# Performance work log

Hardware: AMD Instinct MI355X
Metric: run time of the kernel (lower is better)

Reference implementation:

```python
import jax, jax.numpy as jnp
import numpy as np

NMS_PRE, NMS_POST, NMS_THRESH = 1024, 512, 0.7
B, A, FEAT = 4, 70400, 27648
BN_EPS = 1e-5


def _bev_iou(boxes):
    # boxes: [K, 7] (x, y, z, dx, dy, dz, ry); axis-aligned BEV IoU
    x, y, dx, dy = boxes[:, 0], boxes[:, 1], boxes[:, 3], boxes[:, 4]
    x1, x2 = x - 0.5 * dx, x + 0.5 * dx
    y1, y2 = y - 0.5 * dy, y + 0.5 * dy
    iw = jnp.clip(jnp.minimum(x2[:, None], x2[None, :]) - jnp.maximum(x1[:, None], x1[None, :]), 0.0)
    ih = jnp.clip(jnp.minimum(y2[:, None], y2[None, :]) - jnp.maximum(y1[:, None], y1[None, :]), 0.0)
    inter = iw * ih
    area = dx * dy
    return inter / jnp.clip(area[:, None] + area[None, :] - inter, 1e-6)


def _greedy_nms(boxes, thresh):
    # boxes sorted by score desc; returns keep mask [K]
    K = boxes.shape[0]
    iou = _bev_iou(boxes)
    idx = jnp.arange(K)

    def step(keep, i):
        sup = (iou[i] > thresh) & (idx > i) & keep[i]
        return keep & ~sup, None

    keep, _ = jax.lax.scan(step, jnp.ones(K, dtype=bool), jnp.arange(K))
    return keep


def _proposal_one(box, cls):
    # box: [A, 7], cls: [A, n_cls]  ->  padded rois [NPOST,7], scores [NPOST], labels [NPOST]
    score = jnp.max(cls, axis=-1)
    label = jnp.argmax(cls, axis=-1)
    top_score, top_idx = jax.lax.top_k(score, NMS_PRE)
    top_box = box[top_idx]
    keep = _greedy_nms(top_box, NMS_THRESH)
    # stable: kept entries first, preserving score order
    order = jnp.argsort(jnp.where(keep, jnp.arange(NMS_PRE), NMS_PRE + jnp.arange(NMS_PRE)))
    sel = order[:NMS_POST]
    valid = jnp.arange(NMS_POST) < jnp.minimum(jnp.sum(keep), NMS_POST)
    rois = jnp.where(valid[:, None], top_box[sel], 0.0)
    roi_score = jnp.where(valid, top_score[sel], 0.0)
    roi_label = jnp.where(valid, label[top_idx][sel], 0) + 1  # +1 as in module
    return rois, roi_score, roi_label


def _bn_relu(h, g, b):
    # eval-mode BN with running_mean=0, running_var=1
    return jax.nn.relu(h * (g / jnp.sqrt(1.0 + BN_EPS)) + b)


def _decode(reg, anchors):
    # ResidualCoder_v1.decode_torch
    xa, ya, za = anchors[..., 0], anchors[..., 1], anchors[..., 2]
    dxa, dya, dza, ra = anchors[..., 3], anchors[..., 4], anchors[..., 5], anchors[..., 6]
    xt, yt, zt = reg[..., 0], reg[..., 1], reg[..., 2]
    dxt, dyt, dzt, rt = reg[..., 3], reg[..., 4], reg[..., 5], reg[..., 6]
    diag = jnp.sqrt(dxa * dxa + dya * dya)
    return jnp.stack([
        xt * diag + xa, yt * diag + ya, zt * dza + za,
        jnp.exp(dxt) * dxa, jnp.exp(dyt) * dya, jnp.exp(dzt) * dza,
        rt + ra], axis=-1)


def _rotate_z(box, ang):
    # rotate x,y of box [..., 7] by ang [...]
    c, s = jnp.cos(ang), jnp.sin(ang)
    x = box[..., 0] * c - box[..., 1] * s
    y = box[..., 0] * s + box[..., 1] * c
    return jnp.concatenate([x[..., None], y[..., None], box[..., 2:]], axis=-1)


def reference(rpn_box_preds, rpn_cls_preds, pooled_features,
              Ws1, g1, b1, Ws2, g2, b2,
              Wc1, gc1, bc1, Wc2, gc2, bc2, Wc3, bc3,
              Wr1, gr1, br1, Wr2, gr2, br2, Wr3, br3):
    # proposal_layer: per-batch topk + NMS + padded scatter (vmapped)
    rois, roi_scores, roi_labels = jax.vmap(_proposal_one)(rpn_box_preds, rpn_cls_preds)

    # shared / cls / reg heads (1x1 Conv1d == per-roi MLP), dropout off (eval)
    x = _bn_relu(pooled_features @ Ws1.T, g1, b1)
    x = _bn_relu(x @ Ws2.T, g2, b2)
    c = _bn_relu(x @ Wc1.T, gc1, bc1)
    c = _bn_relu(c @ Wc2.T, gc2, bc2)
    cls_preds = c @ Wc3.T + bc3          # [B*NPOST, 1]
    r = _bn_relu(x @ Wr1.T, gr1, br1)
    r = _bn_relu(r @ Wr2.T, gr2, br2)
    reg_preds = r @ Wr3.T + br3          # [B*NPOST, 7]

    bsz = rois.shape[0]
    cls_preds = cls_preds.reshape(bsz, -1, cls_preds.shape[-1])
    reg_preds = reg_preds.reshape(bsz, -1, 7)

    # generate_predict_box: decode against detached rois with xyz zeroed
    anchors = jax.lax.stop_gradient(rois)
    anchors = anchors.at[..., 0:3].set(0.0)
    box_ct = _decode(reg_preds, anchors)
    box_preds = _rotate_z(box_ct, rois[..., 6])
    box_preds = jnp.concatenate([box_preds[..., 0:3] + rois[..., 0:3], box_preds[..., 3:]], axis=-1)

    return jnp.concatenate([cls_preds, box_preds, roi_scores[..., None]], axis=-1)  # [B, NPOST, 9]


def setup_inputs():
    key = jax.random.key(0)
    ks = jax.random.split(key, 32)
    u = jax.random.uniform(ks[0], (B, A, 7), dtype=jnp.float32)
    lo = jnp.array([0.0, -40.0, -2.0, 1.5, 1.4, 1.0, -3.14159], jnp.float32)
    hi = jnp.array([70.0, 40.0, 0.0, 4.5, 2.0, 2.0, 3.14159], jnp.float32)
    rpn_box_preds = lo + u * (hi - lo)
    rpn_cls_preds = jax.random.normal(ks[1], (B, A, 3), dtype=jnp.float32)
    pooled_features = jax.random.normal(ks[2], (B * NMS_POST, FEAT), dtype=jnp.float32) * 0.1

    def w(k, o, i, std=None):
        s = (1.0 / np.sqrt(i)) if std is None else std
        return jax.random.normal(k, (o, i), dtype=jnp.float32) * s

    d = dict(
        rpn_box_preds=rpn_box_preds, rpn_cls_preds=rpn_cls_preds, pooled_features=pooled_features,
        Ws1=w(ks[3], 256, FEAT), g1=jnp.ones(256), b1=jnp.zeros(256),
        Ws2=w(ks[4], 256, 256), g2=jnp.ones(256), b2=jnp.zeros(256),
        Wc1=w(ks[5], 256, 256), gc1=jnp.ones(256), bc1=jnp.zeros(256),
        Wc2=w(ks[6], 256, 256), gc2=jnp.ones(256), bc2=jnp.zeros(256),
        Wc3=w(ks[7], 1, 256), bc3=jnp.zeros(1),
        Wr1=w(ks[8], 256, 256), gr1=jnp.ones(256), br1=jnp.zeros(256),
        Wr2=w(ks[9], 256, 256), gr2=jnp.ones(256), br2=jnp.zeros(256),
        Wr3=w(ks[10], 7, 256, std=0.001), br3=jnp.zeros(7),
    )
    return d
```

## Files before the change

### kernel.cpp

```cpp
#include <hip/hip_runtime.h>
#include <cstdint>

typedef unsigned int u32;
typedef unsigned long long u64;
typedef unsigned short u16;

#define BATCH 4
#define A_CNT 70400
#define FEAT 27648
#define KSPLIT 16
#define KCHUNK 1728
#define NTILE_IT 27

typedef __attribute__((ext_vector_type(8))) short bf16x8;
typedef __attribute__((ext_vector_type(4))) float f32x4;
typedef __attribute__((ext_vector_type(2))) u32 u32x2;
typedef __attribute__((ext_vector_type(4))) u32 u32x4;

constexpr size_t OF_KEYS = 0;
constexpr size_t OF_TBOX = OF_KEYS + 1126400;
constexpr size_t OF_TSC  = OF_TBOX + 114688;
constexpr size_t OF_BX1  = OF_TSC + 16384;
constexpr size_t OF_BX2  = OF_BX1 + 16384;
constexpr size_t OF_BY1  = OF_BX2 + 16384;
constexpr size_t OF_BY2  = OF_BY1 + 16384;
constexpr size_t OF_BAR  = OF_BY2 + 16384;
constexpr size_t OF_MASK = OF_BAR + 16384;
constexpr size_t OF_ROIS = OF_MASK + 524288;
constexpr size_t OF_RSC  = OF_ROIS + 57344;
constexpr size_t OF_BSW  = OF_RSC + 8192;
constexpr size_t OF_PART = OF_BSW + 14155776;
constexpr size_t WS_NEED = OF_PART + 33554432;

__device__ __forceinline__ u32 keyOf(float f) {
  u32 u = __float_as_uint(f);
  return (u & 0x80000000u) ? ~u : (u | 0x80000000u);
}
__device__ __forceinline__ float keyToF(u32 k) {
  u32 u = (k & 0x80000000u) ? (k ^ 0x80000000u) : ~k;
  return __uint_as_float(u);
}
__device__ __forceinline__ u16 f2bf(float f) {
  u32 u = __float_as_uint(f);
  u32 r = 0x7FFFu + ((u >> 16) & 1u);
  return (u16)((u + r) >> 16);
}
__device__ __forceinline__ void gload_lds16(const void* g, void* l) {
  auto gp = reinterpret_cast<const __attribute__((address_space(1))) unsigned int*>(
      reinterpret_cast<uintptr_t>(g));
  auto lp = reinterpret_cast<__attribute__((address_space(3))) unsigned int*>(
      reinterpret_cast<uintptr_t>(l));
  __builtin_amdgcn_global_load_lds(gp, lp, 16, 0, 0);
}
__device__ __forceinline__ u64 shflx64(u64 v, int m) {
  u32 lo = (u32)v, hi = (u32)(v >> 32);
  lo = __shfl_xor(lo, m, 64);
  hi = __shfl_xor(hi, m, 64);
  return ((u64)hi << 32) | lo;
}
__device__ __forceinline__ u32x4 pack8(float4 a, float4 b) {
  u32x4 o;
  o.x = (u32)f2bf(a.x) | ((u32)f2bf(a.y) << 16);
  o.y = (u32)f2bf(a.z) | ((u32)f2bf(a.w) << 16);
  o.z = (u32)f2bf(b.x) | ((u32)f2bf(b.y) << 16);
  o.w = (u32)f2bf(b.z) | ((u32)f2bf(b.w) << 16);
  return o;
}

__global__ __launch_bounds__(1024) void k_fatA(const float* __restrict__ cls,
    const float* __restrict__ Ws1, u32* __restrict__ keys, u32* __restrict__ Bsw)
{
  int bid = blockIdx.x;
  int t = threadIdx.x;
  if (bid < 864) {
    u32 w = (u32)bid * 1024u + t;
    u32 tile = w >> 11;
    u32 rem = w & 2047u;
    u32 n = rem >> 3;
    u32 pq = (rem & 7u) << 4;
    u32 q0 = pq ^ ((n & 7u) << 4);
    u32 col0 = tile * 64u + (q0 >> 1);
    const float* src = Ws1 + (size_t)n * FEAT + col0;
    float4 f0 = *(const float4*)src;
    float4 f1 = *(const float4*)(src + 4);
    ((u32x4*)Bsw)[w] = pack8(f0, f1);
    return;
  }
  u32 g = (u32)(bid - 864) * 1024u + t;
  float s0 = cls[(size_t)g * 3 + 0];
  float s1 = cls[(size_t)g * 3 + 1];
  float s2 = cls[(size_t)g * 3 + 2];
  keys[g] = keyOf(fmaxf(s0, fmaxf(s1, s2)));
}

__global__ __launch_bounds__(1024) void k_big(const u32* __restrict__ keys,
    const float* __restrict__ boxes, const float* __restrict__ A,
    const u32* __restrict__ Bsw, float* __restrict__ part,
    float* __restrict__ tbox, float* __restrict__ tsc,
    float* __restrict__ bx1, float* __restrict__ bx2, float* __restrict__ by1,
    float* __restrict__ by2, float* __restrict__ bar)
{
  __shared__ __align__(16) char smem[81920];
  int bid = blockIdx.x;
  int t = threadIdx.x;
  if (bid < 4) {
    int b = bid;
    int lane = t & 63, wv = t >> 6;
    const u32* kb = keys + (size_t)b * A_CNT;
    u64* s = (u64*)smem;
    u32* partials = (u32*)(smem + 16384);
    u32* ccp = (u32*)(smem + 16448);
    u32 h[35];
#pragma unroll
    for (int j = 0; j < 35; ++j) {
      int g0 = t + ((2 * j) << 10);
      int g1 = t + ((2 * j + 1) << 10);
      u32 a = (g0 < A_CNT) ? (kb[g0] >> 16) : 0u;
      u32 c2 = (g1 < A_CNT) ? (kb[g1] >> 16) : 0u;
      h[j] = a | (c2 << 16);
    }
    if (t == 0) ccp[0] = 0u;
    u32 lo = 0, hi = 65536;
    while (hi - lo > 1) {
      u32 mid = (lo + hi) >> 1;
      u32 c = 0;
#pragma unroll
      for (int j = 0; j < 35; ++j) {
        c += ((h[j] & 0xFFFFu) >= mid) ? 1u : 0u;
        c += ((h[j] >> 16) >= mid) ? 1u : 0u;
      }
#pragma unroll
      for (int o = 32; o > 0; o >>= 1) c += __shfl_xor(c, o, 64);
      __syncthreads();
      if (lane == 0) partials[wv] = c;
      __syncthreads();
      u32 tot = 0;
#pragma unroll
      for (int w2 = 0; w2 < 16; ++w2) tot += partials[w2];
      if (tot >= 1024u) lo = mid; else hi = mid;
    }
    u32 kth = lo;
    __syncthreads();
    u32 kc = kb[t];
#pragma unroll 1
    for (int i = 0; i < 69; ++i) {
      int g = t + (i << 10);
      u32 k = kc;
      if (i < 68) {
        int gn = t + ((i + 1) << 10);
        kc = (gn < A_CNT) ? kb[gn] : 0u;
      }
      bool pass = (g < A_CNT) && ((k >> 16) >= kth);
      u64 mm = __ballot(pass);
      if (mm) {
        int leader = __ffsll((unsigned long long)mm) - 1;
        u32 base = 0;
        if (lane == leader) base = atomicAdd(ccp, (u32)__popcll(mm));
        base = __shfl(base, leader, 64);
        if (pass) {
          u32 pos = base + (u32)__popcll(mm & ((1ull << lane) - 1ull));
          if (pos < 2048u) s[pos] = ((u64)k << 32) | (u32)(~(u32)g);
        }
      }
    }
    __syncthreads();
    u32 m = ccp[0]; if (m > 2048u) m = 2048u;
    for (int e = t; e < 2048; e += 1024) if (e >= (int)m) s[e] = 0ull;
    __syncthreads();
    {
      u64 v0 = s[2 * t], v1 = s[2 * t + 1];
#pragma unroll
      for (u32 k = 2; k <= 128; k <<= 1) {
        bool desc = ((t & (k >> 1)) == 0);
#pragma unroll
        for (u32 j = (k >> 1); j >= 2; j >>= 1) {
          u32 mmk = j >> 1;
          u64 p0 = shflx64(v0, mmk);
          u64 p1 = shflx64(v1, mmk);
          bool up = ((t & mmk) == 0);
          bool mx = (desc == up);
          v0 = mx ? (v0 > p0 ? v0 : p0) : (v0 < p0 ? v0 : p0);
          v1 = mx ? (v1 > p1 ? v1 : p1) : (v1 < p1 ? v1 : p1);
        }
        if (desc ? (v0 < v1) : (v0 > v1)) { u64 tmp = v0; v0 = v1; v1 = tmp; }
      }
      s[2 * t] = v0; s[2 * t + 1] = v1;
      __syncthreads();
      for (u32 k = 256; k <= 2048; k <<= 1) {
        for (u32 j = k >> 1; j >= 128; j >>= 1) {
          for (int e = t; e < 2048; e += 1024) {
            u32 p = (u32)e ^ j;
            if (p > (u32)e) {
              bool d2 = ((e & k) == 0);
              u64 x = s[e], y = s[p];
              if (d2 ? (x < y) : (x > y)) { s[e] = y; s[p] = x; }
            }
          }
          __syncthreads();
        }
        u64 v0 = s[2 * t], v1 = s[2 * t + 1];
        bool desc = ((t & (k >> 1)) == 0);
#pragma unroll
        for (u32 j = 64; j >= 2; j >>= 1) {
          u32 mmk = j >> 1;
          u64 p0 = shflx64(v0, mmk);
          u64 p1 = shflx64(v1, mmk);
          bool up = ((t & mmk) == 0);
          bool mx = (desc == up);
          v0 = mx ? (v0 > p0 ? v0 : p0) : (v0 < p0 ? v0 : p0);
          v1 = mx ? (v1 > p1 ? v1 : p1) : (v1 < p1 ? v1 : p1);
        }
        if (desc ? (v0 < v1) : (v0 > v1)) { u64 tmp = v0; v0 = v1; v1 = tmp; }
        s[2 * t] = v0; s[2 * t + 1] = v1;
        __syncthreads();
      }
    }
    u64 comp = s[t];
    u32 kk = (u32)(comp >> 32);
    u32 a = ~(u32)(comp & 0xFFFFFFFFull);
    int o = b * 1024 + t;
    tsc[o] = keyToF(kk);
    const float* bp = boxes + ((size_t)b * A_CNT + a) * 7;
    float x = bp[0], y = bp[1], z = bp[2], dx = bp[3], dy = bp[4], dz = bp[5], rr = bp[6];
    float* tb = tbox + (size_t)o * 7;
    tb[0] = x; tb[1] = y; tb[2] = z; tb[3] = dx; tb[4] = dy; tb[5] = dz; tb[6] = rr;
    {
#pragma clang fp contract(off)
      bx1[o] = x - 0.5f * dx; bx2[o] = x + 0.5f * dx;
      by1[o] = y - 0.5f * dy; by2[o] = y + 0.5f * dy;
      bar[o] = dx * dy;
    }
    return;
  }
  int bid2 = bid - 4;
  int q = bid2 >> 3;
  int ks = (bid2 & 7) * 2 + (q >> 5);
  int mt = q & 31;
  int lane = t & 63, wvid = t >> 6;
  int row16 = lane & 15, kgrp = lane >> 4;

  f32x4 acc[4];
#pragma unroll
  for (int i = 0; i < 4; ++i) acc[i] = (f32x4){0.f, 0.f, 0.f, 0.f};

  int arow = t >> 4;
  const float* ap_base = A + ((size_t)(mt * 64 + arow)) * FEAT + (size_t)ks * KCHUNK + (t & 15) * 4;
  int asw = (arow & 7) << 4;
  int awoff = arow * 128 + (((t & 15) * 8) ^ asw);
  const char* bsrc_base = (const char*)Bsw + ((size_t)(ks * NTILE_IT)) * 32768 + wvid * 2048 + lane * 16;
  int bdoff = wvid * 2048 + lane * 16;
  char* Abase = smem;
  char* Bbase = smem + 16384;

  int aoff[4][2], boff[2];
#pragma unroll
  for (int ksub = 0; ksub < 2; ++ksub) {
    int qq = ksub * 64 + kgrp * 16;
#pragma unroll
    for (int mf = 0; mf < 4; ++mf) {
      int row = mf * 16 + row16;
      aoff[mf][ksub] = row * 128 + (qq ^ ((row & 7) << 4));
    }
    int n = wvid * 16 + row16;
    boff[ksub] = n * 128 + (qq ^ ((n & 7) << 4));
  }

  {
    float4 ga = *(const float4*)ap_base;
    u32x2 c;
    c.x = (u32)f2bf(ga.x) | ((u32)f2bf(ga.y) << 16);
    c.y = (u32)f2bf(ga.z) | ((u32)f2bf(ga.w) << 16);
    *(u32x2*)(Abase + awoff) = c;
    gload_lds16(bsrc_base, Bbase + bdoff);
    gload_lds16(bsrc_base + 1024, Bbase + bdoff + 1024);
  }
  __syncthreads();

  for (int it = 0; it < NTILE_IT; ++it) {
    char* Acur = Abase + ((it & 1) ? 8192 : 0);
    char* Anxt = Abase + ((it & 1) ? 0 : 8192);
    char* Bcur = Bbase + ((it & 1) ? 32768 : 0);
    char* Bnxt = Bbase + ((it & 1) ? 0 : 32768);
    bool has = (it + 1 < NTILE_IT);
    float4 ga;
    if (has) {
      ga = *(const float4*)(ap_base + (it + 1) * 64);
      const char* bs = bsrc_base + (size_t)(it + 1) * 32768;
      gload_lds16(bs, Bnxt + bdoff);
      gload_lds16(bs + 1024, Bnxt + bdoff + 1024);
    }
    bf16x8 bf0 = *(const bf16x8*)(Bcur + boff[0]);
    bf16x8 bf1 = *(const bf16x8*)(Bcur + boff[1]);
#pragma unroll
    for (int mf = 0; mf < 4; ++mf) {
      bf16x8 a0 = *(const bf16x8*)(Acur + aoff[mf][0]);
      acc[mf] = __builtin_amdgcn_mfma_f32_16x16x32_bf16(a0, bf0, acc[mf], 0, 0, 0);
      bf16x8 a1 = *(const bf16x8*)(Acur + aoff[mf][1]);
      acc[mf] = __builtin_amdgcn_mfma_f32_16x16x32_bf16(a1, bf1, acc[mf], 0, 0, 0);
    }
    if (has) {
      u32x2 c;
      c.x = (u32)f2bf(ga.x) | ((u32)f2bf(ga.y) << 16);
      c.y = (u32)f2bf(ga.z) | ((u32)f2bf(ga.w) << 16);
      *(u32x2*)(Anxt + awoff) = c;
    }
    __syncthreads();
  }
  float* pb = part + (size_t)ks * 524288;
#pragma unroll
  for (int mf = 0; mf < 4; ++mf) {
    int orow = mt * 64 + mf * 16 + kgrp * 4;
    int col = wvid * 16 + row16;
#pragma unroll
    for (int rr = 0; rr < 4; ++rr)
      pb[(size_t)(orow + rr) * 256 + col] = acc[mf][rr];
  }
}

__global__ __launch_bounds__(1024) void k_mask(const float* __restrict__ bx1,
    const float* __restrict__ bx2, const float* __restrict__ by1,
    const float* __restrict__ by2, const float* __restrict__ bar,
    u32* __restrict__ mask)
{
  __shared__ float csm[16][5][64];
  int tt = threadIdx.x;
  int ug = tt >> 6, ln = tt & 63;
  int unit = blockIdx.x * 16 + ug;
  int b = unit >> 8, cbk = (unit >> 4) & 15, rb = unit & 15;
  int o = b * 1024, jc0 = cbk * 64;
  int r = rb * 64 + ln;
  csm[ug][0][ln] = bx1[o + jc0 + ln];
  csm[ug][1][ln] = bx2[o + jc0 + ln];
  csm[ug][2][ln] = by1[o + jc0 + ln];
  csm[ug][3][ln] = by2[o + jc0 + ln];
  csm[ug][4][ln] = bar[o + jc0 + ln];
  __syncthreads();
  float rx1 = bx1[o + r], rx2 = bx2[o + r], ry1 = by1[o + r], ry2 = by2[o + r], rar = bar[o + r];
  u32 w0 = 0, w1 = 0;
  {
#pragma clang fp contract(off)
    for (int c = 0; c < 64; ++c) {
      int jc = jc0 + c;
      float iw = fminf(rx2, csm[ug][1][c]) - fmaxf(rx1, csm[ug][0][c]); iw = fmaxf(iw, 0.0f);
      float ih = fminf(ry2, csm[ug][3][c]) - fmaxf(ry1, csm[ug][2][c]); ih = fmaxf(ih, 0.0f);
      float inter = iw * ih;
      float den = fmaxf(rar + csm[ug][4][c] - inter, 1e-6f);
      float iou = inter / den;
      if ((iou > 0.7f) && (jc > r)) {
        if (c < 32) w0 |= 1u << c; else w1 |= 1u << (c - 32);
      }
    }
  }
  mask[((size_t)(o + r)) * 32 + cbk * 2 + 0] = w0;
  mask[((size_t)(o + r)) * 32 + cbk * 2 + 1] = w1;
}

__global__ __launch_bounds__(64) void k_nms(const u32* __restrict__ mask,
    const float* __restrict__ tbox, const float* __restrict__ tsc,
    float* __restrict__ rois, float* __restrict__ rsc)
{
  int b = blockIdx.x;
  int lane = threadIdx.x;
  int el = lane & 31;
  const u32* M = mask + (size_t)b * 1024 * 32;
  u32 R = 0;
  u32 cur[32], nxt[32];
#pragma unroll
  for (int i = 0; i < 32; ++i) cur[i] = M[(size_t)(i * 32 + el)];
#pragma unroll 1
  for (int c = 0; c < 32; ++c) {
    if (c < 31) {
      int nb = (c + 1) * 1024 + el;
#pragma unroll
      for (int i = 0; i < 32; ++i) nxt[i] = M[(size_t)(nb + i * 32)];
    }
    u32 w = R;
#pragma unroll
    for (int i = 0; i < 32; ++i) w |= ((w >> i) & 1u) ? 0u : cur[i];
    u32 wfin = __shfl(w, c, 64);
#pragma unroll
    for (int i = 0; i < 32; ++i) R |= ((wfin >> i) & 1u) ? 0u : cur[i];
#pragma unroll
    for (int i = 0; i < 32; ++i) cur[i] = nxt[i];
  }
  u32 keepw = (lane < 32) ? ~R : 0u;
  int c = __popc(keepw);
  int pre = c;
  for (int d = 1; d < 64; d <<= 1) {
    int v = __shfl_up(pre, d, 64);
    if (lane >= d) pre += v;
  }
  int total = __shfl(pre, 31, 64);
  int base = pre - c;
  if (lane < 32) {
    u32 w = keepw;
    int rank = base;
    while (w) {
      int bit = __ffs(w) - 1;
      w &= w - 1;
      if (rank < 512) {
        int r = lane * 32 + bit;
        const float* tb = tbox + ((size_t)b * 1024 + r) * 7;
        float* rp = rois + ((size_t)b * 512 + rank) * 7;
        rp[0] = tb[0]; rp[1] = tb[1]; rp[2] = tb[2]; rp[3] = tb[3];
        rp[4] = tb[4]; rp[5] = tb[5]; rp[6] = tb[6];
        rsc[b * 512 + rank] = tsc[b * 1024 + r];
      }
      rank++;
    }
  }
  for (int z = total + lane; z < 512; z += 64) {
    float* rp = rois + ((size_t)b * 512 + z) * 7;
    rp[0] = rp[1] = rp[2] = rp[3] = rp[4] = rp[5] = rp[6] = 0.0f;
    rsc[b * 512 + z] = 0.0f;
  }
}

__device__ __forceinline__ void layer4(const float (*IN)[256], const float* __restrict__ W,
    const float* __restrict__ g, const float* __restrict__ bb, float (*OUT)[256], int t, int h)
{
  float acc[4] = {0, 0, 0, 0};
  const float* Wrow = W + (size_t)t * 256;
  for (int k = 0; k < 256; k += 4) {
    float4 w4 = *(const float4*)&Wrow[k];
#pragma unroll
    for (int r = 0; r < 4; ++r) {
      float4 xv = *(const float4*)&IN[h * 4 + r][k];
      acc[r] = fmaf(xv.x, w4.x, acc[r]);
      acc[r] = fmaf(xv.y, w4.y, acc[r]);
      acc[r] = fmaf(xv.z, w4.z, acc[r]);
      acc[r] = fmaf(xv.w, w4.w, acc[r]);
    }
  }
  float sc = g[t] / sqrtf(1.0f + 1e-5f);
  float bv = bb[t];
#pragma unroll
  for (int r = 0; r < 4; ++r)
    OUT[h * 4 + r][t] = fmaxf(fmaf(acc[r], sc, bv), 0.0f);
}

__global__ __launch_bounds__(512) void k_chain(const float* __restrict__ part,
    const float* __restrict__ Ws2, const float* __restrict__ Wc1, const float* __restrict__ Wc2,
    const float* __restrict__ Wr1, const float* __restrict__ Wr2,
    const float* __restrict__ g1, const float* __restrict__ b1,
    const float* __restrict__ g2, const float* __restrict__ b2,
    const float* __restrict__ gc1, const float* __restrict__ bc1,
    const float* __restrict__ gc2, const float* __restrict__ bc2,
    const float* __restrict__ gr1, const float* __restrict__ br1,
    const float* __restrict__ gr2, const float* __restrict__ br2,
    const float* __restrict__ Wc3, const float* __restrict__ bc3,
    const float* __restrict__ Wr3, const float* __restrict__ br3,
    const float* __restrict__ rois, const float* __restrict__ rsc,
    float* __restrict__ out)
{
  int bid = blockIdx.x, tid = threadIdx.x;
  int t = tid & 255, h = tid >> 8;
  __shared__ __align__(16) float bufX[8][256];
  __shared__ __align__(16) float bufY[8][256];
  __shared__ __align__(16) float bufC[8][256];
  __shared__ __align__(16) float bufR[8][256];
  __shared__ float hd[64];
  {
    float sc = g1[t] / sqrtf(1.0f + 1e-5f);
    float bv = b1[t];
#pragma unroll
    for (int r = 0; r < 4; ++r) {
      int row = h * 4 + r;
      float s = 0.f;
#pragma unroll
      for (int ks = 0; ks < KSPLIT; ++ks)
        s += part[(size_t)ks * 524288 + (size_t)(bid * 8 + row) * 256 + t];
      bufX[row][t] = fmaxf(fmaf(s, sc, bv), 0.0f);
    }
  }
  __syncthreads();
  layer4(bufX, Ws2, g2, b2, bufY, t, h);
  __syncthreads();
  layer4(bufY, Wc1, gc1, bc1, bufC, t, h);
  layer4(bufY, Wr1, gr1, br1, bufR, t, h);
  __syncthreads();
  layer4(bufC, Wc2, gc2, bc2, bufX, t, h);
  layer4(bufR, Wr2, gr2, br2, bufY, t, h);
  __syncthreads();
  int wv = tid >> 6, ln = tid & 63;
  for (int task = wv; task < 64; task += 8) {
    float p;
    if (task < 8) {
      float4 yv = *(const float4*)&bufX[task][ln * 4];
      float4 w4 = ((const float4*)Wc3)[ln];
      p = yv.x * w4.x + yv.y * w4.y + yv.z * w4.z + yv.w * w4.w;
    } else {
      int i = task - 8, row = i / 7, j = i % 7;
      float4 yv = *(const float4*)&bufY[row][ln * 4];
      float4 w4 = ((const float4*)(Wr3 + j * 256))[ln];
      p = yv.x * w4.x + yv.y * w4.y + yv.z * w4.z + yv.w * w4.w;
    }
#pragma unroll
    for (int off = 32; off > 0; off >>= 1) p += __shfl_xor(p, off, 64);
    if (ln == 0) hd[task] = p;
  }
  __syncthreads();
  if (tid < 8) {
    int m = bid * 8 + tid;
    float clsv = hd[tid] + bc3[0];
    float rg[7];
#pragma unroll
    for (int j = 0; j < 7; ++j) rg[j] = hd[8 + tid * 7 + j] + br3[j];
    const float* R = rois + (size_t)m * 7;
    float rx = R[0], ry = R[1], rz = R[2], dxa = R[3], dya = R[4], dza = R[5], ra = R[6];
    float diag = sqrtf(dxa * dxa + dya * dya);
    float x = rg[0] * diag, y = rg[1] * diag, z = rg[2] * dza;
    float ex = expf(rg[3]) * dxa, ey = expf(rg[4]) * dya, ez = expf(rg[5]) * dza;
    float hr = rg[6] + ra;
    float cc = cosf(ra), sn = sinf(ra);
    float xr = x * cc - y * sn, yr = x * sn + y * cc;
    float* O = out + (size_t)m * 9;
    O[0] = clsv; O[1] = xr + rx; O[2] = yr + ry; O[3] = z + rz;
    O[4] = ex; O[5] = ey; O[6] = ez; O[7] = hr; O[8] = rsc[m];
  }
}

extern "C" void kernel_launch(void* const* d_in, const int* in_sizes, int n_in,
                              void* d_out, int out_size, void* d_ws, size_t ws_size,
                              hipStream_t stream)
{
  const float* rpn_box = (const float*)d_in[0];
  const float* rpn_cls = (const float*)d_in[1];
  const float* pooled  = (const float*)d_in[2];
  const float* Ws1 = (const float*)d_in[3];
  const float* g1  = (const float*)d_in[4];
  const float* b1  = (const float*)d_in[5];
  const float* Ws2 = (const float*)d_in[6];
  const float* g2  = (const float*)d_in[7];
  const float* b2  = (const float*)d_in[8];
  const float* Wc1 = (const float*)d_in[9];
  const float* gc1 = (const float*)d_in[10];
  const float* bc1 = (const float*)d_in[11];
  const float* Wc2 = (const float*)d_in[12];
  const float* gc2 = (const float*)d_in[13];
  const float* bc2 = (const float*)d_in[14];
  const float* Wc3 = (const float*)d_in[15];
  const float* bc3 = (const float*)d_in[16];
  const float* Wr1 = (const float*)d_in[17];
  const float* gr1 = (const float*)d_in[18];
  const float* br1 = (const float*)d_in[19];
  const float* Wr2 = (const float*)d_in[20];
  const float* gr2 = (const float*)d_in[21];
  const float* br2 = (const float*)d_in[22];
  const float* Wr3 = (const float*)d_in[23];
  const float* br3 = (const float*)d_in[24];

  if (ws_size < WS_NEED) return;

  char* ws = (char*)d_ws;
  u32* keys = (u32*)(ws + OF_KEYS);
  float* tbox = (float*)(ws + OF_TBOX);
  float* tsc  = (float*)(ws + OF_TSC);
  float* bx1 = (float*)(ws + OF_BX1);
  float* bx2 = (float*)(ws + OF_BX2);
  float* by1 = (float*)(ws + OF_BY1);
  float* by2 = (float*)(ws + OF_BY2);
  float* bar = (float*)(ws + OF_BAR);
  u32* mask = (u32*)(ws + OF_MASK);
  float* roisb = (float*)(ws + OF_ROIS);
  float* rscb  = (float*)(ws + OF_RSC);
  u32* Bsw = (u32*)(ws + OF_BSW);
  float* part = (float*)(ws + OF_PART);

  k_fatA<<<1139, 1024, 0, stream>>>(rpn_cls, Ws1, keys, Bsw);
  k_big<<<516, 1024, 0, stream>>>(keys, rpn_box, pooled, Bsw, part,
                                  tbox, tsc, bx1, bx2, by1, by2, bar);
  k_mask<<<64, 1024, 0, stream>>>(bx1, bx2, by1, by2, bar, mask);
  k_nms<<<4, 64, 0, stream>>>(mask, tbox, tsc, roisb, rscb);
  k_chain<<<256, 512, 0, stream>>>(part, Ws2, Wc1, Wc2, Wr1, Wr2,
                                   g1, b1, g2, b2, gc1, bc1, gc2, bc2,
                                   gr1, br1, gr2, br2, Wc3, bc3, Wr3, br3,
                                   roisb, rscb, (float*)d_out);
}
```

Measured before the change: 251.7 us.

## Enlarge GEMM block tile to 128 rows with 2x4 MFMA fragments per wave

The split-K GEMM blocks in k_big now cover 128 rows of pooled features instead of 64. Each wave computes a 32x64 output sub-tile (2x4 MFMA fragments) rather than 16x64, so every B tile loaded into LDS is reused across twice as many rows. This halves the number of GEMM blocks, and with them the redundant B-matrix global-to-LDS traffic. The cost is more accumulator registers, more LDS (96KB), and fewer blocks (256 GEMM blocks), which can reduce occupancy and parallelism across the GPU.

```diff
diff --git a/kernel.cpp b/kernel.cpp
--- a/kernel.cpp
+++ b/kernel.cpp
@@ -100,7 +100,7 @@
     float* __restrict__ bx1, float* __restrict__ bx2, float* __restrict__ by1,
     float* __restrict__ by2, float* __restrict__ bar)
 {
-  __shared__ __align__(16) char smem[81920];
+  __shared__ __align__(16) char smem[98304];
   int bid = blockIdx.x;
   int t = threadIdx.x;
   if (bid < 4) {
@@ -234,86 +234,96 @@
   }
   int bid2 = bid - 4;
   int q = bid2 >> 3;
-  int ks = (bid2 & 7) * 2 + (q >> 5);
-  int mt = q & 31;
+  int ks = (bid2 & 7) * 2 + (q >> 4);
+  int mt = q & 15;
   int lane = t & 63, wvid = t >> 6;
   int row16 = lane & 15, kgrp = lane >> 4;
-
-  f32x4 acc[4];
-#pragma unroll
-  for (int i = 0; i < 4; ++i) acc[i] = (f32x4){0.f, 0.f, 0.f, 0.f};
-
-  int arow = t >> 4;
-  const float* ap_base = A + ((size_t)(mt * 64 + arow)) * FEAT + (size_t)ks * KCHUNK + (t & 15) * 4;
+  int gm = wvid >> 2, gn = wvid & 3;
+
+  f32x4 acc[2][4];
+#pragma unroll
+  for (int i = 0; i < 2; ++i)
+#pragma unroll
+    for (int j = 0; j < 4; ++j) acc[i][j] = (f32x4){0.f, 0.f, 0.f, 0.f};
+
+  int arow = t >> 3;
+  const float* ap_base = A + ((size_t)(mt * 128 + arow)) * FEAT + (size_t)ks * KCHUNK + (t & 7) * 8;
   int asw = (arow & 7) << 4;
-  int awoff = arow * 128 + (((t & 15) * 8) ^ asw);
+  int awoff = arow * 128 + (((t & 7) * 16) ^ asw);
   const char* bsrc_base = (const char*)Bsw + ((size_t)(ks * NTILE_IT)) * 32768 + wvid * 2048 + lane * 16;
   int bdoff = wvid * 2048 + lane * 16;
   char* Abase = smem;
-  char* Bbase = smem + 16384;
-
-  int aoff[4][2], boff[2];
+  char* Bbase = smem + 32768;
+
+  int aoff[2][2], boff[4][2];
 #pragma unroll
   for (int ksub = 0; ksub < 2; ++ksub) {
     int qq = ksub * 64 + kgrp * 16;
 #pragma unroll
-    for (int mf = 0; mf < 4; ++mf) {
-      int row = mf * 16 + row16;
+    for (int mf = 0; mf < 2; ++mf) {
+      int row = gm * 32 + mf * 16 + row16;
       aoff[mf][ksub] = row * 128 + (qq ^ ((row & 7) << 4));
     }
-    int n = wvid * 16 + row16;
-    boff[ksub] = n * 128 + (qq ^ ((n & 7) << 4));
+#pragma unroll
+    for (int nf = 0; nf < 4; ++nf) {
+      int n = gn * 64 + nf * 16 + row16;
+      boff[nf][ksub] = n * 128 + (qq ^ ((n & 7) << 4));
+    }
   }
 
   {
-    float4 ga = *(const float4*)ap_base;
-    u32x2 c;
-    c.x = (u32)f2bf(ga.x) | ((u32)f2bf(ga.y) << 16);
-    c.y = (u32)f2bf(ga.z) | ((u32)f2bf(ga.w) << 16);
-    *(u32x2*)(Abase + awoff) = c;
+    const float4* ap = (const float4*)ap_base;
+    float4 ga0 = ap[0], ga1 = ap[1];
+    *(u32x4*)(Abase + awoff) = pack8(ga0, ga1);
     gload_lds16(bsrc_base, Bbase + bdoff);
     gload_lds16(bsrc_base + 1024, Bbase + bdoff + 1024);
   }
   __syncthreads();
 
   for (int it = 0; it < NTILE_IT; ++it) {
-    char* Acur = Abase + ((it & 1) ? 8192 : 0);
-    char* Anxt = Abase + ((it & 1) ? 0 : 8192);
+    char* Acur = Abase + ((it & 1) ? 16384 : 0);
+    char* Anxt = Abase + ((it & 1) ? 0 : 16384);
     char* Bcur = Bbase + ((it & 1) ? 32768 : 0);
     char* Bnxt = Bbase + ((it & 1) ? 0 : 32768);
     bool has = (it + 1 < NTILE_IT);
-    float4 ga;
+    float4 ga0, ga1;
     if (has) {
-      ga = *(const float4*)(ap_base + (it + 1) * 64);
+      const float4* ap = (const float4*)(ap_base + (it + 1) * 64);
+      ga0 = ap[0]; ga1 = ap[1];
       const char* bs = bsrc_base + (size_t)(it + 1) * 32768;
       gload_lds16(bs, Bnxt + bdoff);
       gload_lds16(bs + 1024, Bnxt + bdoff + 1024);
     }
-    bf16x8 bf0 = *(const bf16x8*)(Bcur + boff[0]);
-    bf16x8 bf1 = *(const bf16x8*)(Bcur + boff[1]);
-#pragma unroll
-    for (int mf = 0; mf < 4; ++mf) {
-      bf16x8 a0 = *(const bf16x8*)(Acur + aoff[mf][0]);
-      acc[mf] = __builtin_amdgcn_mfma_f32_16x16x32_bf16(a0, bf0, acc[mf], 0, 0, 0);
-      bf16x8 a1 = *(const bf16x8*)(Acur + aoff[mf][1]);
-      acc[mf] = __builtin_amdgcn_mfma_f32_16x16x32_bf16(a1, bf1, acc[mf], 0, 0, 0);
-    }
-    if (has) {
-      u32x2 c;
-      c.x = (u32)f2bf(ga.x) | ((u32)f2bf(ga.y) << 16);
-      c.y = (u32)f2bf(ga.z) | ((u32)f2bf(ga.w) << 16);
-      *(u32x2*)(Anxt + awoff) = c;
-    }
+    bf16x8 af[2][2], bf[4][2];
+#pragma unroll
+    for (int ksub = 0; ksub < 2; ++ksub) {
+#pragma unroll
+      for (int mf = 0; mf < 2; ++mf) af[mf][ksub] = *(const bf16x8*)(Acur + aoff[mf][ksub]);
+#pragma unroll
+      for (int nf = 0; nf < 4; ++nf) bf[nf][ksub] = *(const bf16x8*)(Bcur + boff[nf][ksub]);
+    }
+#pragma unroll
+    for (int ksub = 0; ksub < 2; ++ksub)
+#pragma unroll
+      for (int mf = 0; mf < 2; ++mf)
+#pragma unroll
+        for (int nf = 0; nf < 4; ++nf)
+          acc[mf][nf] = __builtin_amdgcn_mfma_f32_16x16x32_bf16(af[mf][ksub], bf[nf][ksub], acc[mf][nf], 0, 0, 0);
+    if (has)
+      *(u32x4*)(Anxt + awoff) = pack8(ga0, ga1);
     __syncthreads();
   }
   float* pb = part + (size_t)ks * 524288;
 #pragma unroll
-  for (int mf = 0; mf < 4; ++mf) {
-    int orow = mt * 64 + mf * 16 + kgrp * 4;
-    int col = wvid * 16 + row16;
-#pragma unroll
-    for (int rr = 0; rr < 4; ++rr)
-      pb[(size_t)(orow + rr) * 256 + col] = acc[mf][rr];
+  for (int mf = 0; mf < 2; ++mf) {
+    int orow = mt * 128 + gm * 32 + mf * 16 + kgrp * 4;
+#pragma unroll
+    for (int nf = 0; nf < 4; ++nf) {
+      int col = gn * 64 + nf * 16 + row16;
+#pragma unroll
+      for (int rr = 0; rr < 4; ++rr)
+        pb[(size_t)(orow + rr) * 256 + col] = acc[mf][nf][rr];
+    }
   }
 }
 
@@ -568,7 +578,7 @@
   float* part = (float*)(ws + OF_PART);
 
   k_fatA<<<1139, 1024, 0, stream>>>(rpn_cls, Ws1, keys, Bsw);
-  k_big<<<516, 1024, 0, stream>>>(keys, rpn_box, pooled, Bsw, part,
+  k_big<<<260, 1024, 0, stream>>>(keys, rpn_box, pooled, Bsw, part,
                                   tbox, tsc, bx1, bx2, by1, by2, bar);
   k_mask<<<64, 1024, 0, stream>>>(bx1, bx2, by1, by2, bar, mask);
   k_nms<<<4, 64, 0, stream>>>(mask, tbox, tsc, roisb, rscb);
```

Result: no change. 247.2 us (-1.8%).
